# Optimization experiments

Measured on AMD Instinct MI355X. Metric: run time of the kernel, lower is better.

The kernel has to match this reference:

```python
import jax, jax.numpy as jnp
import numpy as np

B, C, H, W = 16, 1, 2048, 128
K8 = 8  # conv1/conv2 expand in_dim -> in_dim*8 channels


def setup_inputs() -> dict:
    key = jax.random.key(0)
    k = jax.random.split(key, 6)
    x = jax.random.normal(k[0], (B, C, H, W), dtype=jnp.float32)
    # 1x1 convs with in_channels=1 reduce to per-output-channel scale + bias
    w1 = jax.random.normal(k[1], (K8,), dtype=jnp.float32) * 0.5
    b1 = jax.random.normal(k[2], (K8,), dtype=jnp.float32) * 0.1
    w2 = jax.random.normal(k[3], (K8,), dtype=jnp.float32) * 0.5
    b2 = jax.random.normal(k[4], (K8,), dtype=jnp.float32) * 0.1
    gamma = jax.random.normal(k[5], (1,), dtype=jnp.float32) * 0.1
    return {"x": x, "w1": w1, "b1": b1, "w2": w2, "b2": b2, "gamma": gamma}


def reference(x, w1, b1, w2, b2, gamma):
    # x: (B,1,H,W)
    # conv1 / conv2: 1x1 conv, 1 -> 8 channels == scale+bias broadcast
    p1 = x * w1[None, :, None, None] + b1[None, :, None, None]  # (B,8,H,W)
    p2 = x * w2[None, :, None, None] + b2[None, :, None, None]  # (B,8,H,W)
    # proj_query: permute(0,2,1,3).reshape(B,H,8W)
    q = p1.transpose(0, 2, 1, 3).reshape(B, H, K8 * W)
    # proj_key: permute(0,1,3,2).reshape(B,8W,H)
    k_ = p2.transpose(0, 1, 3, 2).reshape(B, K8 * W, H)
    energy = jnp.einsum('bhd,bdg->bhg', q, k_)  # (B,H,H)
    mn = energy.min(axis=2, keepdims=True)
    mx = energy.max(axis=2, keepdims=True)
    energy = (energy - mn) / (mx - mn + 1e-8)
    attn = jax.nn.softmax(energy, axis=2)  # (B,H,H)
    # attention.reshape(B,1,H,H) @ x (B,1,H,W) -> (B,1,H,W)
    out = jnp.einsum('bhg,bgw->bhw', attn, x[:, 0])[:, None]
    return gamma * out + x
```

## Files before the change

### kernel.cpp

```cpp
#include <hip/hip_runtime.h>
#include <hip/hip_bf16.h>

#define B_ 16
#define H_ 2048
#define W_ 128

using f32x4  = __attribute__((ext_vector_type(4))) float;
using bf16x8 = __attribute__((ext_vector_type(8))) short;

#define GLOAD_LDS16(g, l) __builtin_amdgcn_global_load_lds( \
    (const __attribute__((address_space(1))) unsigned int*)(g), \
    (__attribute__((address_space(3))) unsigned int*)(l), 16, 0, 0)

__device__ inline short bf16bits(float f) {
    union { __hip_bfloat16 h; short s; } u;
    u.h = __float2bfloat16(f);
    return u.s;
}

__global__ __launch_bounds__(256) void prep(const float* __restrict__ x,
                                            const float* __restrict__ b1,
                                            const float* __restrict__ w2,
                                            __hip_bfloat16* __restrict__ Xbt,
                                            __hip_bfloat16* __restrict__ XTt,
                                            float* __restrict__ cs) {
    __shared__ float xs[64][136];
    __shared__ float psum[64][4];
    int b  = blockIdx.x >> 5;
    int g0 = (blockIdx.x & 31) * 64;
    const float* xb = x + ((size_t)b * H_ + g0) * W_;
    int t = threadIdx.x;
    {
        int col = (t & 31) * 4, r0 = t >> 5;
#pragma unroll
        for (int p = 0; p < 8; ++p) {
            int row = p * 8 + r0;
            float4 v = *reinterpret_cast<const float4*>(xb + (size_t)row * W_ + col);
            *reinterpret_cast<float4*>(&xs[row][col]) = v;
        }
    }
    __syncthreads();
    {
        int row = t >> 2, quad = t & 3;
        float sum = 0.f;
#pragma unroll
        for (int j = 0; j < 32; ++j) sum += xs[row][quad * 32 + j];
        psum[row][quad] = sum;
    }
    __syncthreads();
    if (t < 64) {
        float C = 0.f;
#pragma unroll
        for (int c = 0; c < 8; ++c) C += b1[c] * w2[c];
        float s = psum[t][0] + psum[t][1] + psum[t][2] + psum[t][3];
        cs[b * H_ + g0 + t] = C * s;
    }
    {
        __hip_bfloat16* outb = Xbt + (size_t)b * H_ * W_ + (size_t)g0 * W_;
#pragma unroll
        for (int it = 0; it < 4; ++it) {
            int c = it * 256 + t;
            int r = c & 15, q = (c >> 4) & 3, k = (c >> 6) & 3, gbl = c >> 8;
            const float* src = &xs[gbl * 16 + r][k * 32 + q * 8];
            float4 v0 = *reinterpret_cast<const float4*>(src);
            float4 v1 = *reinterpret_cast<const float4*>(src + 4);
            bf16x8 v;
            v[0] = bf16bits(v0.x); v[1] = bf16bits(v0.y);
            v[2] = bf16bits(v0.z); v[3] = bf16bits(v0.w);
            v[4] = bf16bits(v1.x); v[5] = bf16bits(v1.y);
            v[6] = bf16bits(v1.z); v[7] = bf16bits(v1.w);
            *reinterpret_cast<bf16x8*>(outb + (size_t)c * 8) = v;
        }
    }
    {
        __hip_bfloat16* outt = XTt + (size_t)b * H_ * W_ + (size_t)g0 * W_;
#pragma unroll
        for (int it = 0; it < 4; ++it) {
            int c = it * 256 + t;
            int r = c & 15, q = (c >> 4) & 3, nt2 = (c >> 6) & 7, kt = (c >> 9) & 1;
            bf16x8 v;
#pragma unroll
            for (int j = 0; j < 8; ++j)
                v[j] = bf16bits(xs[kt * 32 + q * 8 + j][nt2 * 16 + r]);
            *reinterpret_cast<bf16x8*>(outt + (size_t)c * 8) = v;
        }
    }
}

__global__ __launch_bounds__(256, 2) void fused_attn(
    const float* __restrict__ x,
    const __hip_bfloat16* __restrict__ Xbt, const __hip_bfloat16* __restrict__ XTt,
    const float* __restrict__ cs,
    const float* __restrict__ w1, const float* __restrict__ w2,
    const float* __restrict__ gamma, float* __restrict__ out) {
    __shared__ __align__(16) char stgA[2][16384];
    __shared__ __align__(16) char stgV[2][16384];
    __shared__ __align__(16) char pb[4][2048];

    float A = 0.f;
#pragma unroll
    for (int c = 0; c < 8; ++c) A += w1[c] * w2[c];

    int wave = threadIdx.x >> 6, lane = threadIdx.x & 63;
    int q = lane >> 4, r = lane & 15;

    int bid = blockIdx.x;
    int swz = (bid & 7) * 64 + (bid >> 3);
    int b  = swz >> 5;
    int hb = swz & 31;
    int h0 = hb * 64 + wave * 16;

    const char* xbt = (const char*)(Xbt + (size_t)b * H_ * W_);
    const char* xtt = (const char*)(XTt + (size_t)b * H_ * W_);
    const float* csb = cs + b * H_;

    bf16x8 afr[4];
#pragma unroll
    for (int k = 0; k < 4; ++k)
        afr[k] = *reinterpret_cast<const bf16x8*>(
            xbt + (((size_t)(h0 >> 4) * 4 + k) * 64 + lane) * 16);

    float mnv[4], mxv[4];
#pragma unroll
    for (int i = 0; i < 4; ++i) { mnv[i] = 3.4e38f; mxv[i] = -3.4e38f; }

    {
        const char* ga = xbt + wave * 4096 + lane * 16;
        char* la = stgA[0] + wave * 4096;
#pragma unroll
        for (int i = 0; i < 4; ++i) GLOAD_LDS16(ga + i * 1024, la + i * 1024);
    }
    __syncthreads();
    for (int t = 0; t < 32; ++t) {
        int cur = t & 1;
        if (t < 31) {
            const char* ga = xbt + (size_t)(t + 1) * 16384 + wave * 4096 + lane * 16;
            char* la = stgA[cur ^ 1] + wave * 4096;
#pragma unroll
            for (int i = 0; i < 4; ++i) GLOAD_LDS16(ga + i * 1024, la + i * 1024);
        }
        const char* sa = stgA[cur] + lane * 16;
#pragma unroll
        for (int gbl = 0; gbl < 4; ++gbl) {
            f32x4 acc = {0.f, 0.f, 0.f, 0.f};
#pragma unroll
            for (int k = 0; k < 4; ++k) {
                bf16x8 bfr = *reinterpret_cast<const bf16x8*>(sa + ((gbl * 4 + k) * 64) * 16);
                acc = __builtin_amdgcn_mfma_f32_16x16x32_bf16(afr[k], bfr, acc, 0, 0, 0);
            }
            float sg = csb[t * 64 + gbl * 16 + r];
#pragma unroll
            for (int reg = 0; reg < 4; ++reg) {
                float tv = fmaf(A, acc[reg], sg);
                mnv[reg] = fminf(mnv[reg], tv);
                mxv[reg] = fmaxf(mxv[reg], tv);
            }
        }
        __syncthreads();
    }
#pragma unroll
    for (int reg = 0; reg < 4; ++reg) {
#pragma unroll
        for (int m = 1; m < 16; m <<= 1) {
            mnv[reg] = fminf(mnv[reg], __shfl_xor(mnv[reg], m, 64));
            mxv[reg] = fmaxf(mxv[reg], __shfl_xor(mxv[reg], m, 64));
        }
    }
    const float LOG2E = 1.4426950408889634f;
    float c1[4], c0v[4];
#pragma unroll
    for (int reg = 0; reg < 4; ++reg) {
        float inv = LOG2E / (mxv[reg] - mnv[reg] + 1e-8f);
        c1[reg]  = inv;
        c0v[reg] = -mnv[reg] * inv;
    }

    f32x4 o[8];
#pragma unroll
    for (int i = 0; i < 8; ++i) o[i] = (f32x4){0.f, 0.f, 0.f, 0.f};
    float zacc[4] = {0.f, 0.f, 0.f, 0.f};

    {
        const char* ga = xbt + wave * 4096 + lane * 16;
        char* la = stgA[0] + wave * 4096;
        const char* gv = xtt + wave * 4096 + lane * 16;
        char* lv = stgV[0] + wave * 4096;
#pragma unroll
        for (int i = 0; i < 4; ++i) {
            GLOAD_LDS16(ga + i * 1024, la + i * 1024);
            GLOAD_LDS16(gv + i * 1024, lv + i * 1024);
        }
    }
    __syncthreads();
    char* pw = pb[wave];
    for (int t = 0; t < 32; ++t) {
        int cur = t & 1;
        if (t < 31) {
            const char* ga = xbt + (size_t)(t + 1) * 16384 + wave * 4096 + lane * 16;
            char* la = stgA[cur ^ 1] + wave * 4096;
            const char* gv = xtt + (size_t)(t + 1) * 16384 + wave * 4096 + lane * 16;
            char* lv = stgV[cur ^ 1] + wave * 4096;
#pragma unroll
            for (int i = 0; i < 4; ++i) {
                GLOAD_LDS16(ga + i * 1024, la + i * 1024);
                GLOAD_LDS16(gv + i * 1024, lv + i * 1024);
            }
        }
        const char* sa = stgA[cur] + lane * 16;
        const char* sv = stgV[cur] + lane * 16;
#pragma unroll
        for (int gbl = 0; gbl < 4; ++gbl) {
            f32x4 acc = {0.f, 0.f, 0.f, 0.f};
#pragma unroll
            for (int k = 0; k < 4; ++k) {
                bf16x8 bfr = *reinterpret_cast<const bf16x8*>(sa + ((gbl * 4 + k) * 64) * 16);
                acc = __builtin_amdgcn_mfma_f32_16x16x32_bf16(afr[k], bfr, acc, 0, 0, 0);
            }
            float sg = csb[t * 64 + gbl * 16 + r];
            int kt = gbl >> 1;
            int qq = ((gbl & 1) << 1) | (r >> 3);
            int jb = (r & 7) * 2;
#pragma unroll
            for (int reg = 0; reg < 4; ++reg) {
                float tv = fmaf(A, acc[reg], sg);
                float e = exp2f(fmaf(tv, c1[reg], c0v[reg]));
                zacc[reg] += e;
                int h = q * 4 + reg;
                *reinterpret_cast<short*>(pw + (kt * 64 + qq * 16 + h) * 16 + jb) = bf16bits(e);
            }
        }
#pragma unroll
        for (int kt = 0; kt < 2; ++kt) {
            bf16x8 pa = *reinterpret_cast<const bf16x8*>(pw + kt * 1024 + lane * 16);
#pragma unroll
            for (int nt2 = 0; nt2 < 8; ++nt2) {
                bf16x8 btf = *reinterpret_cast<const bf16x8*>(sv + ((kt * 8 + nt2) * 64) * 16);
                o[nt2] = __builtin_amdgcn_mfma_f32_16x16x32_bf16(pa, btf, o[nt2], 0, 0, 0);
            }
        }
        __syncthreads();
    }

#pragma unroll
    for (int reg = 0; reg < 4; ++reg) {
#pragma unroll
        for (int m = 1; m < 16; m <<= 1) zacc[reg] += __shfl_xor(zacc[reg], m, 64);
    }

    float g_ = gamma[0];
    const float* xrow = x + (size_t)b * H_ * W_;
    float* orow = out + (size_t)b * H_ * W_;
#pragma unroll
    for (int reg = 0; reg < 4; ++reg) {
        float sc = g_ / zacc[reg];
        int h = h0 + q * 4 + reg;
#pragma unroll
        for (int nt2 = 0; nt2 < 8; ++nt2) {
            int w = nt2 * 16 + r;
            size_t idx = (size_t)h * W_ + w;
            orow[idx] = fmaf(sc, o[nt2][reg], xrow[idx]);
        }
    }
}

extern "C" void kernel_launch(void* const* d_in, const int* in_sizes, int n_in,
                              void* d_out, int out_size, void* d_ws, size_t ws_size,
                              hipStream_t stream) {
    const float* x     = (const float*)d_in[0];
    const float* w1    = (const float*)d_in[1];
    const float* b1    = (const float*)d_in[2];
    const float* w2    = (const float*)d_in[3];
    const float* b2    = (const float*)d_in[4];
    const float* gamma = (const float*)d_in[5];
    float* out = (float*)d_out;
    (void)b2;

    char* ws = (char*)d_ws;
    const size_t XB_BYTES = (size_t)B_ * H_ * W_ * 2;
    __hip_bfloat16* Xbt = (__hip_bfloat16*)ws;
    __hip_bfloat16* XTt = (__hip_bfloat16*)(ws + XB_BYTES);
    float* cs = (float*)(ws + 2 * XB_BYTES);

    prep<<<B_ * 32, 256, 0, stream>>>(x, b1, w2, Xbt, XTt, cs);
    fused_attn<<<B_ * H_ / 64, 256, 0, stream>>>(x, Xbt, XTt, cs, w1, w2, gamma, out);
}
```

Baseline: 171.0 us.

## Split attention block into 2x2 wave grid over rows and key columns with smaller tiles

The fused attention kernel now arranges its four waves as a 2x2 grid. Each wave covers 32 query rows and half of the key/value column chunk, so every LDS B-fragment feeds two MFMAs. Staging tiles are halved to 32 keys per step, and min/max and softmax denominators are reduced across wave pairs through shared memory. The probability tile is shared across waves and needs an extra barrier per step. The prep kernel is also rewritten to convert to bf16 directly from global memory into a swizzled bf16 LDS tile, cutting LDS footprint and bank conflicts.

Result: slower. 178.6 us (+4.4%).

```diff
diff --git a/kernel.cpp b/kernel.cpp
--- a/kernel.cpp
+++ b/kernel.cpp
@@ -21,244 +21,250 @@
 __global__ __launch_bounds__(256) void prep(const float* __restrict__ x,
                                             const float* __restrict__ b1,
                                             const float* __restrict__ w2,
-                                            __hip_bfloat16* __restrict__ Xbt,
-                                            __hip_bfloat16* __restrict__ XTt,
+                                            short* __restrict__ Xbt,
+                                            short* __restrict__ XTt,
                                             float* __restrict__ cs) {
-    __shared__ float xs[64][136];
-    __shared__ float psum[64][4];
+    __shared__ short xs2[8192];
     int b  = blockIdx.x >> 5;
     int g0 = (blockIdx.x & 31) * 64;
     const float* xb = x + ((size_t)b * H_ + g0) * W_;
-    int t = threadIdx.x;
-    {
-        int col = (t & 31) * 4, r0 = t >> 5;
-#pragma unroll
-        for (int p = 0; p < 8; ++p) {
-            int row = p * 8 + r0;
-            float4 v = *reinterpret_cast<const float4*>(xb + (size_t)row * W_ + col);
-            *reinterpret_cast<float4*>(&xs[row][col]) = v;
-        }
-    }
-    __syncthreads();
-    {
-        int row = t >> 2, quad = t & 3;
-        float sum = 0.f;
-#pragma unroll
-        for (int j = 0; j < 32; ++j) sum += xs[row][quad * 32 + j];
-        psum[row][quad] = sum;
-    }
-    __syncthreads();
-    if (t < 64) {
-        float C = 0.f;
-#pragma unroll
-        for (int c = 0; c < 8; ++c) C += b1[c] * w2[c];
-        float s = psum[t][0] + psum[t][1] + psum[t][2] + psum[t][3];
-        cs[b * H_ + g0 + t] = C * s;
-    }
-    {
-        __hip_bfloat16* outb = Xbt + (size_t)b * H_ * W_ + (size_t)g0 * W_;
-#pragma unroll
-        for (int it = 0; it < 4; ++it) {
-            int c = it * 256 + t;
-            int r = c & 15, q = (c >> 4) & 3, k = (c >> 6) & 3, gbl = c >> 8;
-            const float* src = &xs[gbl * 16 + r][k * 32 + q * 8];
-            float4 v0 = *reinterpret_cast<const float4*>(src);
-            float4 v1 = *reinterpret_cast<const float4*>(src + 4);
-            bf16x8 v;
-            v[0] = bf16bits(v0.x); v[1] = bf16bits(v0.y);
-            v[2] = bf16bits(v0.z); v[3] = bf16bits(v0.w);
-            v[4] = bf16bits(v1.x); v[5] = bf16bits(v1.y);
-            v[6] = bf16bits(v1.z); v[7] = bf16bits(v1.w);
-            *reinterpret_cast<bf16x8*>(outb + (size_t)c * 8) = v;
-        }
-    }
-    {
-        __hip_bfloat16* outt = XTt + (size_t)b * H_ * W_ + (size_t)g0 * W_;
-#pragma unroll
-        for (int it = 0; it < 4; ++it) {
-            int c = it * 256 + t;
-            int r = c & 15, q = (c >> 4) & 3, nt2 = (c >> 6) & 7, kt = (c >> 9) & 1;
-            bf16x8 v;
-#pragma unroll
-            for (int j = 0; j < 8; ++j)
-                v[j] = bf16bits(xs[kt * 32 + q * 8 + j][nt2 * 16 + r]);
-            *reinterpret_cast<bf16x8*>(outt + (size_t)c * 8) = v;
-        }
+    short* outb = Xbt + (size_t)b * H_ * W_ + (size_t)g0 * W_;
+    short* outt = XTt + (size_t)b * H_ * W_ + (size_t)g0 * W_;
+    int t = threadIdx.x, seg = t & 15, row_l = t >> 4;
+    float Cc = 0.f;
+#pragma unroll
+    for (int c = 0; c < 8; ++c) Cc += b1[c] * w2[c];
+
+#pragma unroll
+    for (int it = 0; it < 4; ++it) {
+        int row = it * 16 + row_l;
+        const float* src = xb + (size_t)row * W_ + seg * 8;
+        float4 v0 = *reinterpret_cast<const float4*>(src);
+        float4 v1 = *reinterpret_cast<const float4*>(src + 4);
+        bf16x8 v;
+        v[0] = bf16bits(v0.x); v[1] = bf16bits(v0.y);
+        v[2] = bf16bits(v0.z); v[3] = bf16bits(v0.w);
+        v[4] = bf16bits(v1.x); v[5] = bf16bits(v1.y);
+        v[6] = bf16bits(v1.z); v[7] = bf16bits(v1.w);
+        int chunk = (it * 4 + (seg >> 2)) * 64 + (seg & 3) * 16 + row_l;
+        *reinterpret_cast<bf16x8*>(outb + (size_t)chunk * 8) = v;
+        float s = v0.x + v0.y + v0.z + v0.w + v1.x + v1.y + v1.z + v1.w;
+        s += __shfl_xor(s, 1); s += __shfl_xor(s, 2);
+        s += __shfl_xor(s, 4); s += __shfl_xor(s, 8);
+        if (seg == 0) cs[b * H_ + g0 + row] = Cc * s;
+        int c8 = seg ^ ((row >> 3) & 3);
+        *reinterpret_cast<bf16x8*>(&xs2[row * 128 + c8 * 8]) = v;
+    }
+    __syncthreads();
+#pragma unroll
+    for (int it2 = 0; it2 < 4; ++it2) {
+        int c = it2 * 256 + t;
+        int r = c & 15, qp = (c >> 4) & 3, nt2 = (c >> 6) & 7, kt = c >> 9;
+        int w = nt2 * 16 + r, g = kt * 32 + qp * 8;
+        int c8p = (w >> 3) ^ ((g >> 3) & 3);
+        bf16x8 vv;
+#pragma unroll
+        for (int jj = 0; jj < 8; ++jj)
+            vv[jj] = xs2[(g + jj) * 128 + c8p * 8 + (w & 7)];
+        *reinterpret_cast<bf16x8*>(outt + (size_t)c * 8) = vv;
     }
 }
 
 __global__ __launch_bounds__(256, 2) void fused_attn(
     const float* __restrict__ x,
-    const __hip_bfloat16* __restrict__ Xbt, const __hip_bfloat16* __restrict__ XTt,
+    const short* __restrict__ Xbt, const short* __restrict__ XTt,
     const float* __restrict__ cs,
     const float* __restrict__ w1, const float* __restrict__ w2,
     const float* __restrict__ gamma, float* __restrict__ out) {
-    __shared__ __align__(16) char stgA[2][16384];
-    __shared__ __align__(16) char stgV[2][16384];
-    __shared__ __align__(16) char pb[4][2048];
+    __shared__ __align__(16) char stgA[2][8192];
+    __shared__ __align__(16) char stgV[2][8192];
+    __shared__ __align__(16) char pb[2][4096];
+    __shared__ float red_mn[2][2][2][16];
+    __shared__ float red_mx[2][2][2][16];
+    __shared__ float zred[2][2][2][16];
 
     float A = 0.f;
 #pragma unroll
     for (int c = 0; c < 8; ++c) A += w1[c] * w2[c];
 
-    int wave = threadIdx.x >> 6, lane = threadIdx.x & 63;
+    int tid = threadIdx.x;
+    int wv = tid >> 6, lane = tid & 63;
+    int wh = wv >> 1, wg = wv & 1;
     int q = lane >> 4, r = lane & 15;
 
     int bid = blockIdx.x;
     int swz = (bid & 7) * 64 + (bid >> 3);
-    int b  = swz >> 5;
-    int hb = swz & 31;
-    int h0 = hb * 64 + wave * 16;
+    int b = swz >> 5, hb = swz & 31;
+    int h_base = hb * 64;
 
     const char* xbt = (const char*)(Xbt + (size_t)b * H_ * W_);
     const char* xtt = (const char*)(XTt + (size_t)b * H_ * W_);
     const float* csb = cs + b * H_;
 
-    bf16x8 afr[4];
-#pragma unroll
-    for (int k = 0; k < 4; ++k)
-        afr[k] = *reinterpret_cast<const bf16x8*>(
-            xbt + (((size_t)(h0 >> 4) * 4 + k) * 64 + lane) * 16);
-
-    float mnv[4], mxv[4];
-#pragma unroll
-    for (int i = 0; i < 4; ++i) { mnv[i] = 3.4e38f; mxv[i] = -3.4e38f; }
-
+    bf16x8 afr[2][4];
+#pragma unroll
+    for (int hf = 0; hf < 2; ++hf)
+#pragma unroll
+        for (int k = 0; k < 4; ++k)
+            afr[hf][k] = *reinterpret_cast<const bf16x8*>(
+                xbt + (((size_t)((h_base >> 4) + wh * 2 + hf) * 4 + k) * 64 + lane) * 16);
+
+    float mnv[2] = {3.4e38f, 3.4e38f}, mxv[2] = {-3.4e38f, -3.4e38f};
     {
-        const char* ga = xbt + wave * 4096 + lane * 16;
-        char* la = stgA[0] + wave * 4096;
-#pragma unroll
-        for (int i = 0; i < 4; ++i) GLOAD_LDS16(ga + i * 1024, la + i * 1024);
-    }
-    __syncthreads();
-    for (int t = 0; t < 32; ++t) {
-        int cur = t & 1;
-        if (t < 31) {
-            const char* ga = xbt + (size_t)(t + 1) * 16384 + wave * 4096 + lane * 16;
-            char* la = stgA[cur ^ 1] + wave * 4096;
-#pragma unroll
-            for (int i = 0; i < 4; ++i) GLOAD_LDS16(ga + i * 1024, la + i * 1024);
-        }
-        const char* sa = stgA[cur] + lane * 16;
-#pragma unroll
-        for (int gbl = 0; gbl < 4; ++gbl) {
-            f32x4 acc = {0.f, 0.f, 0.f, 0.f};
-#pragma unroll
-            for (int k = 0; k < 4; ++k) {
-                bf16x8 bfr = *reinterpret_cast<const bf16x8*>(sa + ((gbl * 4 + k) * 64) * 16);
-                acc = __builtin_amdgcn_mfma_f32_16x16x32_bf16(afr[k], bfr, acc, 0, 0, 0);
+        const char* ga = xbt + wv * 2048 + lane * 16;
+        char* la = stgA[0] + wv * 2048;
+        GLOAD_LDS16(ga, la); GLOAD_LDS16(ga + 1024, la + 1024);
+    }
+    __syncthreads();
+    float4 csv = *reinterpret_cast<const float4*>(csb + wg * 16 + q * 4);
+    for (int t = 0; t < 64; ++t) {
+        float4 csn = csv;
+        if (t < 63) {
+            const char* ga = xbt + (size_t)(t + 1) * 8192 + wv * 2048 + lane * 16;
+            char* la = stgA[(t + 1) & 1] + wv * 2048;
+            GLOAD_LDS16(ga, la); GLOAD_LDS16(ga + 1024, la + 1024);
+            csn = *reinterpret_cast<const float4*>(csb + (t + 1) * 32 + wg * 16 + q * 4);
+        }
+        const char* sa = stgA[t & 1] + lane * 16;
+        bf16x8 bfr[4];
+#pragma unroll
+        for (int k = 0; k < 4; ++k)
+            bfr[k] = *reinterpret_cast<const bf16x8*>(sa + ((wg * 4 + k) * 64) * 16);
+        f32x4 s0 = {0.f, 0.f, 0.f, 0.f}, s1 = {0.f, 0.f, 0.f, 0.f};
+#pragma unroll
+        for (int k = 0; k < 4; ++k) {
+            s0 = __builtin_amdgcn_mfma_f32_16x16x32_bf16(bfr[k], afr[0][k], s0, 0, 0, 0);
+            s1 = __builtin_amdgcn_mfma_f32_16x16x32_bf16(bfr[k], afr[1][k], s1, 0, 0, 0);
+        }
+#pragma unroll
+        for (int reg = 0; reg < 4; ++reg) {
+            float t0 = fmaf(A, s0[reg], csv[reg]);
+            float t1 = fmaf(A, s1[reg], csv[reg]);
+            mnv[0] = fminf(mnv[0], t0); mxv[0] = fmaxf(mxv[0], t0);
+            mnv[1] = fminf(mnv[1], t1); mxv[1] = fmaxf(mxv[1], t1);
+        }
+        __syncthreads();
+        csv = csn;
+    }
+#pragma unroll
+    for (int hf = 0; hf < 2; ++hf) {
+        mnv[hf] = fminf(mnv[hf], __shfl_xor(mnv[hf], 16));
+        mnv[hf] = fminf(mnv[hf], __shfl_xor(mnv[hf], 32));
+        mxv[hf] = fmaxf(mxv[hf], __shfl_xor(mxv[hf], 16));
+        mxv[hf] = fmaxf(mxv[hf], __shfl_xor(mxv[hf], 32));
+    }
+    if (lane < 16) {
+        red_mn[wh][0][wg][lane] = mnv[0]; red_mn[wh][1][wg][lane] = mnv[1];
+        red_mx[wh][0][wg][lane] = mxv[0]; red_mx[wh][1][wg][lane] = mxv[1];
+    }
+    __syncthreads();
+    const float LOG2E = 1.4426950408889634f;
+    float c1[2], c0v[2], A1[2];
+#pragma unroll
+    for (int hf = 0; hf < 2; ++hf) {
+        float mn = fminf(red_mn[wh][hf][0][r], red_mn[wh][hf][1][r]);
+        float mx = fmaxf(red_mx[wh][hf][0][r], red_mx[wh][hf][1][r]);
+        float inv = LOG2E / (mx - mn + 1e-8f);
+        c1[hf] = inv; c0v[hf] = -mn * inv; A1[hf] = A * inv;
+    }
+
+    f32x4 o[2][4];
+#pragma unroll
+    for (int i = 0; i < 2; ++i)
+#pragma unroll
+        for (int j = 0; j < 4; ++j) o[i][j] = (f32x4){0.f, 0.f, 0.f, 0.f};
+    float zacc[2] = {0.f, 0.f};
+    {
+        const char* ga = xbt + wv * 2048 + lane * 16;
+        char* la = stgA[0] + wv * 2048;
+        const char* gv = xtt + wv * 2048 + lane * 16;
+        char* lv = stgV[0] + wv * 2048;
+        GLOAD_LDS16(ga, la); GLOAD_LDS16(ga + 1024, la + 1024);
+        GLOAD_LDS16(gv, lv); GLOAD_LDS16(gv + 1024, lv + 1024);
+    }
+    __syncthreads();
+    csv = *reinterpret_cast<const float4*>(csb + wg * 16 + q * 4);
+    for (int t = 0; t < 64; ++t) {
+        float4 csn = csv;
+        if (t < 63) {
+            const char* ga = xbt + (size_t)(t + 1) * 8192 + wv * 2048 + lane * 16;
+            char* la = stgA[(t + 1) & 1] + wv * 2048;
+            const char* gv = xtt + (size_t)(t + 1) * 8192 + wv * 2048 + lane * 16;
+            char* lv = stgV[(t + 1) & 1] + wv * 2048;
+            GLOAD_LDS16(ga, la); GLOAD_LDS16(ga + 1024, la + 1024);
+            GLOAD_LDS16(gv, lv); GLOAD_LDS16(gv + 1024, lv + 1024);
+            csn = *reinterpret_cast<const float4*>(csb + (t + 1) * 32 + wg * 16 + q * 4);
+        }
+        const char* sa = stgA[t & 1] + lane * 16;
+        bf16x8 bfr[4];
+#pragma unroll
+        for (int k = 0; k < 4; ++k)
+            bfr[k] = *reinterpret_cast<const bf16x8*>(sa + ((wg * 4 + k) * 64) * 16);
+        const char* sv = stgV[t & 1] + lane * 16;
+        bf16x8 bt[4];
+#pragma unroll
+        for (int n = 0; n < 4; ++n)
+            bt[n] = *reinterpret_cast<const bf16x8*>(sv + (((wg * 4 + n)) * 64) * 16);
+        f32x4 s0 = {0.f, 0.f, 0.f, 0.f}, s1 = {0.f, 0.f, 0.f, 0.f};
+#pragma unroll
+        for (int k = 0; k < 4; ++k) {
+            s0 = __builtin_amdgcn_mfma_f32_16x16x32_bf16(bfr[k], afr[0][k], s0, 0, 0, 0);
+            s1 = __builtin_amdgcn_mfma_f32_16x16x32_bf16(bfr[k], afr[1][k], s1, 0, 0, 0);
+        }
+        char* pw = pb[t & 1];
+#pragma unroll
+        for (int hf = 0; hf < 2; ++hf) {
+            f32x4 ss = hf ? s1 : s0;
+            float e0 = exp2f(fmaf(ss[0], A1[hf], fmaf(csv[0], c1[hf], c0v[hf])));
+            float e1 = exp2f(fmaf(ss[1], A1[hf], fmaf(csv[1], c1[hf], c0v[hf])));
+            float e2 = exp2f(fmaf(ss[2], A1[hf], fmaf(csv[2], c1[hf], c0v[hf])));
+            float e3 = exp2f(fmaf(ss[3], A1[hf], fmaf(csv[3], c1[hf], c0v[hf])));
+            zacc[hf] += (e0 + e1) + (e2 + e3);
+            unsigned d0 = (unsigned)(unsigned short)bf16bits(e0) |
+                          ((unsigned)(unsigned short)bf16bits(e1) << 16);
+            unsigned d1 = (unsigned)(unsigned short)bf16bits(e2) |
+                          ((unsigned)(unsigned short)bf16bits(e3) << 16);
+            uint2 dd; dd.x = d0; dd.y = d1;
+            *reinterpret_cast<uint2*>(
+                pw + (((wh * 2 + hf) * 64 + (wg * 2 + (q >> 1)) * 16 + r) * 16 + (q & 1) * 8)) = dd;
+        }
+        __syncthreads();
+        bf16x8 pa0 = *reinterpret_cast<const bf16x8*>(pw + ((wh * 2 + 0) * 64 + lane) * 16);
+        bf16x8 pa1 = *reinterpret_cast<const bf16x8*>(pw + ((wh * 2 + 1) * 64 + lane) * 16);
+#pragma unroll
+        for (int n = 0; n < 4; ++n) {
+            o[0][n] = __builtin_amdgcn_mfma_f32_16x16x32_bf16(pa0, bt[n], o[0][n], 0, 0, 0);
+            o[1][n] = __builtin_amdgcn_mfma_f32_16x16x32_bf16(pa1, bt[n], o[1][n], 0, 0, 0);
+        }
+        csv = csn;
+    }
+
+#pragma unroll
+    for (int hf = 0; hf < 2; ++hf) {
+        zacc[hf] += __shfl_xor(zacc[hf], 16);
+        zacc[hf] += __shfl_xor(zacc[hf], 32);
+    }
+    if (lane < 16) {
+        zred[wh][0][wg][lane] = zacc[0];
+        zred[wh][1][wg][lane] = zacc[1];
+    }
+    __syncthreads();
+
+    float g_ = gamma[0];
+#pragma unroll
+    for (int hf = 0; hf < 2; ++hf) {
+#pragma unroll
+        for (int reg = 0; reg < 4; ++reg) {
+            int hq = q * 4 + reg;
+            float z = zred[wh][hf][0][hq] + zred[wh][hf][1][hq];
+            float sc = g_ / z;
+            int h = h_base + wh * 32 + hf * 16 + hq;
+#pragma unroll
+            for (int n = 0; n < 4; ++n) {
+                int w = wg * 64 + n * 16 + r;
+                size_t idx = ((size_t)b * H_ + h) * W_ + w;
+                out[idx] = fmaf(sc, o[hf][n][reg], x[idx]);
             }
-            float sg = csb[t * 64 + gbl * 16 + r];
-#pragma unroll
-            for (int reg = 0; reg < 4; ++reg) {
-                float tv = fmaf(A, acc[reg], sg);
-                mnv[reg] = fminf(mnv[reg], tv);
-                mxv[reg] = fmaxf(mxv[reg], tv);
-            }
-        }
-        __syncthreads();
-    }
-#pragma unroll
-    for (int reg = 0; reg < 4; ++reg) {
-#pragma unroll
-        for (int m = 1; m < 16; m <<= 1) {
-            mnv[reg] = fminf(mnv[reg], __shfl_xor(mnv[reg], m, 64));
-            mxv[reg] = fmaxf(mxv[reg], __shfl_xor(mxv[reg], m, 64));
-        }
-    }
-    const float LOG2E = 1.4426950408889634f;
-    float c1[4], c0v[4];
-#pragma unroll
-    for (int reg = 0; reg < 4; ++reg) {
-        float inv = LOG2E / (mxv[reg] - mnv[reg] + 1e-8f);
-        c1[reg]  = inv;
-        c0v[reg] = -mnv[reg] * inv;
-    }
-
-    f32x4 o[8];
-#pragma unroll
-    for (int i = 0; i < 8; ++i) o[i] = (f32x4){0.f, 0.f, 0.f, 0.f};
-    float zacc[4] = {0.f, 0.f, 0.f, 0.f};
-
-    {
-        const char* ga = xbt + wave * 4096 + lane * 16;
-        char* la = stgA[0] + wave * 4096;
-        const char* gv = xtt + wave * 4096 + lane * 16;
-        char* lv = stgV[0] + wave * 4096;
-#pragma unroll
-        for (int i = 0; i < 4; ++i) {
-            GLOAD_LDS16(ga + i * 1024, la + i * 1024);
-            GLOAD_LDS16(gv + i * 1024, lv + i * 1024);
-        }
-    }
-    __syncthreads();
-    char* pw = pb[wave];
-    for (int t = 0; t < 32; ++t) {
-        int cur = t & 1;
-        if (t < 31) {
-            const char* ga = xbt + (size_t)(t + 1) * 16384 + wave * 4096 + lane * 16;
-            char* la = stgA[cur ^ 1] + wave * 4096;
-            const char* gv = xtt + (size_t)(t + 1) * 16384 + wave * 4096 + lane * 16;
-            char* lv = stgV[cur ^ 1] + wave * 4096;
-#pragma unroll
-            for (int i = 0; i < 4; ++i) {
-                GLOAD_LDS16(ga + i * 1024, la + i * 1024);
-                GLOAD_LDS16(gv + i * 1024, lv + i * 1024);
-            }
-        }
-        const char* sa = stgA[cur] + lane * 16;
-        const char* sv = stgV[cur] + lane * 16;
-#pragma unroll
-        for (int gbl = 0; gbl < 4; ++gbl) {
-            f32x4 acc = {0.f, 0.f, 0.f, 0.f};
-#pragma unroll
-            for (int k = 0; k < 4; ++k) {
-                bf16x8 bfr = *reinterpret_cast<const bf16x8*>(sa + ((gbl * 4 + k) * 64) * 16);
-                acc = __builtin_amdgcn_mfma_f32_16x16x32_bf16(afr[k], bfr, acc, 0, 0, 0);
-            }
-            float sg = csb[t * 64 + gbl * 16 + r];
-            int kt = gbl >> 1;
-            int qq = ((gbl & 1) << 1) | (r >> 3);
-            int jb = (r & 7) * 2;
-#pragma unroll
-            for (int reg = 0; reg < 4; ++reg) {
-                float tv = fmaf(A, acc[reg], sg);
-                float e = exp2f(fmaf(tv, c1[reg], c0v[reg]));
-                zacc[reg] += e;
-                int h = q * 4 + reg;
-                *reinterpret_cast<short*>(pw + (kt * 64 + qq * 16 + h) * 16 + jb) = bf16bits(e);
-            }
-        }
-#pragma unroll
-        for (int kt = 0; kt < 2; ++kt) {
-            bf16x8 pa = *reinterpret_cast<const bf16x8*>(pw + kt * 1024 + lane * 16);
-#pragma unroll
-            for (int nt2 = 0; nt2 < 8; ++nt2) {
-                bf16x8 btf = *reinterpret_cast<const bf16x8*>(sv + ((kt * 8 + nt2) * 64) * 16);
-                o[nt2] = __builtin_amdgcn_mfma_f32_16x16x32_bf16(pa, btf, o[nt2], 0, 0, 0);
-            }
-        }
-        __syncthreads();
-    }
-
-#pragma unroll
-    for (int reg = 0; reg < 4; ++reg) {
-#pragma unroll
-        for (int m = 1; m < 16; m <<= 1) zacc[reg] += __shfl_xor(zacc[reg], m, 64);
-    }
-
-    float g_ = gamma[0];
-    const float* xrow = x + (size_t)b * H_ * W_;
-    float* orow = out + (size_t)b * H_ * W_;
-#pragma unroll
-    for (int reg = 0; reg < 4; ++reg) {
-        float sc = g_ / zacc[reg];
-        int h = h0 + q * 4 + reg;
-#pragma unroll
-        for (int nt2 = 0; nt2 < 8; ++nt2) {
-            int w = nt2 * 16 + r;
-            size_t idx = (size_t)h * W_ + w;
-            orow[idx] = fmaf(sc, o[nt2][reg], xrow[idx]);
         }
     }
 }
@@ -277,9 +283,9 @@
 
     char* ws = (char*)d_ws;
     const size_t XB_BYTES = (size_t)B_ * H_ * W_ * 2;
-    __hip_bfloat16* Xbt = (__hip_bfloat16*)ws;
-    __hip_bfloat16* XTt = (__hip_bfloat16*)(ws + XB_BYTES);
-    float* cs = (float*)(ws + 2 * XB_BYTES);
+    short* Xbt = (short*)ws;
+    short* XTt = (short*)(ws + XB_BYTES);
+    float* cs  = (float*)(ws + 2 * XB_BYTES);
 
     prep<<<B_ * 32, 256, 0, stream>>>(x, b1, w2, Xbt, XTt, cs);
     fused_attn<<<B_ * H_ / 64, 256, 0, stream>>>(x, Xbt, XTt, cs, w1, w2, gamma, out);
```
